# Optimization experiments

Hardware: AMD Instinct MI355X
Metric: run time of the kernel (lower is better)

Reference implementation:

```python
import jax, jax.numpy as jnp
import numpy as np
import math

E = 1024      # embed_dim
H = 16        # num_heads
HD = E // H   # head_dim
NBITS = 8


def fake_quant(x, n_bits=NBITS):
    """Symmetric per-tensor fake quantize with STE (clamp/round/dequant)."""
    qmax = 2.0 ** (n_bits - 1) - 1.0
    qmin = -(2.0 ** (n_bits - 1))
    scale = jnp.maximum(jnp.max(jnp.abs(x)) / qmax, 1e-8)
    xq = jnp.round(jnp.clip(x / scale, qmin, qmax)) * scale
    return x + jax.lax.stop_gradient(xq - x)


def setup_inputs() -> dict:
    key = jax.random.key(0)
    ks = jax.random.split(key, 7)
    L, B = 2048, 2
    query = jax.random.normal(ks[0], (L, B, E), dtype=jnp.float32)
    k_in = jax.random.normal(ks[1], (L, B, E), dtype=jnp.float32)
    v_in = jax.random.normal(ks[2], (L, B, E), dtype=jnp.float32)
    in_w = jax.random.normal(ks[3], (3 * E, E), dtype=jnp.float32) * (1.0 / math.sqrt(E))
    in_b = jax.random.normal(ks[4], (3 * E,), dtype=jnp.float32) * 0.01
    out_w = jax.random.normal(ks[5], (E, E), dtype=jnp.float32) * (1.0 / math.sqrt(E))
    out_b = jax.random.normal(ks[6], (E,), dtype=jnp.float32) * 0.01
    return {"query": query, "key": k_in, "value": v_in,
            "in_w": in_w, "in_b": in_b, "out_w": out_w, "out_b": out_b}


def reference(query, key, value, in_w, in_b, out_w, out_b):
    # NOTE: the original module ignores `key`/`value` (pure self-attention on query),
    # and its attn / softmax fake-quant lines are dead statements (results discarded).
    L, B, _ = query.shape
    Wi = fake_quant(in_w)
    Wo = fake_quant(out_w)
    # input projection: [L,B,3E]
    X = jnp.einsum('lbe,fe->lbf', query, Wi) + in_b
    X = fake_quant(X)
    Q, K, V = jnp.split(X, 3, axis=-1)  # each [L,B,E]
    # [L, B*H, HD] -> [B*H, L, HD]
    q = Q.reshape(L, B * H, HD).transpose(1, 0, 2)
    k = K.reshape(L, B * H, HD).transpose(1, 0, 2)
    v = V.reshape(L, B * H, HD).transpose(1, 0, 2)
    q = q / math.sqrt(HD)
    q = fake_quant(q)
    attn = jnp.einsum('bqd,bkd->bqk', q, k)          # [B*H, L, L]
    attn = jax.nn.softmax(attn, axis=-1)
    heads = jnp.einsum('bqk,bkd->bqd', attn, v)      # [B*H, L, HD]
    heads = fake_quant(heads)
    # [B*H, L, HD] -> [L, B*H, HD] -> [L*B, E]
    heads_r = heads.transpose(1, 0, 2).reshape(L * B, E)
    y = heads_r @ Wo.T + out_b
    y = y.reshape(L, B, E)
    return fake_quant(y)
```

## Files before the change

kernel.cpp:

```cpp
#include <hip/hip_runtime.h>
#include <math.h>

#define L_SEQ 2048
#define BATCH 2
#define EMB 1024
#define NH 16
#define HDIM 64
#define F3 3072
#define NROWS 4096

typedef __bf16 bf16_t;
typedef short s16x8 __attribute__((ext_vector_type(8)));
typedef float f32x4 __attribute__((ext_vector_type(4)));

#define MFMA16(a, b, c) __builtin_amdgcn_mfma_f32_16x16x32_bf16(a, b, c, 0, 0, 0)


__device__ __forceinline__ float u2f(unsigned u) { return __uint_as_float(u); }

__device__ __forceinline__ float max3f(float a, float b, float c) {
  return fmaxf(fmaxf(a, b), c);
}

__device__ __forceinline__ void gload16(const bf16_t* g, bf16_t* lds) {
  __builtin_amdgcn_global_load_lds((const __attribute__((address_space(1))) void*)g,
                                   (__attribute__((address_space(3))) void*)lds, 16, 0, 0);
}

__device__ __forceinline__ void blockmax_commit(float m, unsigned* slot) {
  #pragma unroll
  for (int o = 1; o < 64; o <<= 1) m = fmaxf(m, __shfl_xor(m, o));
  __shared__ float sm_[4];
  if ((threadIdx.x & 63) == 0) sm_[threadIdx.x >> 6] = m;
  __syncthreads();
  if (threadIdx.x == 0) {
    float mm = fmaxf(fmaxf(sm_[0], sm_[1]), fmaxf(sm_[2], sm_[3]));
    atomicMax(slot, __float_as_uint(mm));
  }
}

__global__ __launch_bounds__(256) void wabsmax_k(const float* __restrict__ wi,
                                                 const float* __restrict__ wo,
                                                 unsigned* __restrict__ slots) {
  float m0 = 0.0f, m1 = 0.0f;
  const int n0 = F3 * EMB / 4, n1 = EMB * EMB / 4;
  for (int i = blockIdx.x * blockDim.x + threadIdx.x; i < n0; i += gridDim.x * blockDim.x) {
    float4 v = ((const float4*)wi)[i];
    m0 = fmaxf(m0, fmaxf(fmaxf(fabsf(v.x), fabsf(v.y)), fmaxf(fabsf(v.z), fabsf(v.w))));
  }
  for (int i = blockIdx.x * blockDim.x + threadIdx.x; i < n1; i += gridDim.x * blockDim.x) {
    float4 v = ((const float4*)wo)[i];
    m1 = fmaxf(m1, fmaxf(fmaxf(fabsf(v.x), fabsf(v.y)), fmaxf(fabsf(v.z), fabsf(v.w))));
  }
  blockmax_commit(m0, slots + 0);
  blockmax_commit(m1, slots + 1);
}

__global__ __launch_bounds__(256) void prep_k(const float* __restrict__ wi,
                                              const float* __restrict__ wo,
                                              const float* __restrict__ query,
                                              bf16_t* __restrict__ Wi_int,
                                              bf16_t* __restrict__ Wo_int,
                                              bf16_t* __restrict__ q_hi,
                                              bf16_t* __restrict__ q_lo,
                                              const unsigned* __restrict__ slots) {
  float s0 = fmaxf(u2f(slots[0]) / 127.0f, 1e-8f);
  float s1 = fmaxf(u2f(slots[1]) / 127.0f, 1e-8f);
  const int n0 = F3 * EMB / 4, n1 = EMB * EMB / 4, n2 = NROWS * EMB / 4;
  for (int i = blockIdx.x * blockDim.x + threadIdx.x; i < n0; i += gridDim.x * blockDim.x) {
    float4 v = ((const float4*)wi)[i];
    bf16_t o[4];
    o[0] = (bf16_t)rintf(fminf(fmaxf(v.x / s0, -128.0f), 127.0f));
    o[1] = (bf16_t)rintf(fminf(fmaxf(v.y / s0, -128.0f), 127.0f));
    o[2] = (bf16_t)rintf(fminf(fmaxf(v.z / s0, -128.0f), 127.0f));
    o[3] = (bf16_t)rintf(fminf(fmaxf(v.w / s0, -128.0f), 127.0f));
    *(uint2*)&Wi_int[(size_t)i * 4] = *(uint2*)o;
  }
  for (int i = blockIdx.x * blockDim.x + threadIdx.x; i < n1; i += gridDim.x * blockDim.x) {
    float4 v = ((const float4*)wo)[i];
    bf16_t o[4];
    o[0] = (bf16_t)rintf(fminf(fmaxf(v.x / s1, -128.0f), 127.0f));
    o[1] = (bf16_t)rintf(fminf(fmaxf(v.y / s1, -128.0f), 127.0f));
    o[2] = (bf16_t)rintf(fminf(fmaxf(v.z / s1, -128.0f), 127.0f));
    o[3] = (bf16_t)rintf(fminf(fmaxf(v.w / s1, -128.0f), 127.0f));
    *(uint2*)&Wo_int[(size_t)i * 4] = *(uint2*)o;
  }
  for (int i = blockIdx.x * blockDim.x + threadIdx.x; i < n2; i += gridDim.x * blockDim.x) {
    float4 v = ((const float4*)query)[i];
    bf16_t h[4], l[4];
    float vv[4] = {v.x, v.y, v.z, v.w};
    #pragma unroll
    for (int j = 0; j < 4; ++j) {
      h[j] = (bf16_t)vv[j];
      l[j] = (bf16_t)(vv[j] - (float)h[j]);
    }
    *(uint2*)&q_hi[(size_t)i * 4] = *(uint2*)h;
    *(uint2*)&q_lo[(size_t)i * 4] = *(uint2*)l;
  }
}

__global__ __launch_bounds__(256) void qxv_k(const float* __restrict__ x,
                                             bf16_t* __restrict__ y,
                                             bf16_t* __restrict__ Vt,
                                             unsigned* __restrict__ slots) {
  float s = fmaxf(u2f(slots[2]) / 127.0f, 1e-8f);
  if (blockIdx.x < 2048) {
    float qm = 0.0f;
    const int n8 = NROWS * 256;
    for (int i = blockIdx.x * 256 + threadIdx.x; i < n8; i += 2048 * 256) {
      int row = i >> 8, ch = i & 255;
      const float* px = x + (size_t)row * F3 + ch * 8;
      float4 v0 = *(const float4*)px;
      float4 v1 = *(const float4*)(px + 4);
      float vv[8] = {v0.x, v0.y, v0.z, v0.w, v1.x, v1.y, v1.z, v1.w};
      bf16_t o[8];
      float lm = 0.0f;
      #pragma unroll
      for (int j = 0; j < 8; ++j) {
        float q = rintf(fminf(fmaxf(vv[j] / s, -128.0f), 127.0f));
        o[j] = (bf16_t)q;
        lm = fmaxf(lm, fabsf(q));
      }
      if (ch < 128) qm = fmaxf(qm, lm);
      *(uint4*)&y[(size_t)row * F3 + ch * 8] = *(uint4*)o;
    }
    blockmax_commit(qm, slots + 3);
  } else {
    __shared__ __align__(16) bf16_t tile[64][72];
    int vb = blockIdx.x - 2048;
    int tt = vb & 31, bh = vb >> 5;
    int b = bh >> 4, h = bh & 15;
    int t = threadIdx.x;
    #pragma unroll
    for (int i = 0; i < 2; ++i) {
      int s_ = t + i * 256;
      int tok = s_ >> 3, seg = s_ & 7;
      const float* px = x + ((size_t)(tt * 64 + tok) * BATCH + b) * F3 + 2 * EMB + h * HDIM + seg * 8;
      float4 v0 = *(const float4*)px;
      float4 v1 = *(const float4*)(px + 4);
      float vv[8] = {v0.x, v0.y, v0.z, v0.w, v1.x, v1.y, v1.z, v1.w};
      bf16_t o[8];
      #pragma unroll
      for (int j = 0; j < 8; ++j)
        o[j] = (bf16_t)rintf(fminf(fmaxf(vv[j] / s, -128.0f), 127.0f));
      int segs = seg ^ (tok >> 3);
      *(uint4*)&tile[tok][segs * 8] = *(uint4*)o;
    }
    __syncthreads();
    #pragma unroll
    for (int i = 0; i < 2; ++i) {
      int s_ = t + i * 256;
      int d = s_ >> 3, tseg = s_ & 7;
      bf16_t o[8];
      #pragma unroll
      for (int e = 0; e < 8; ++e) {
        int tok = tseg * 8 + e;
        o[e] = tile[tok][(((d >> 3) ^ (tok >> 3)) << 3) | (d & 7)];
      }
      *(uint4*)&Vt[((size_t)bh * HDIM + d) * L_SEQ + tt * 64 + tseg * 8] = *(uint4*)o;
    }
  }
}

__global__ __launch_bounds__(256) void quant_k(float* __restrict__ x, int n4,
                                               const unsigned* __restrict__ slots, int sloti) {
  float s = fmaxf(u2f(slots[sloti]) / 127.0f, 1e-8f);
  float4* x4 = (float4*)x;
  for (int i = blockIdx.x * blockDim.x + threadIdx.x; i < n4; i += gridDim.x * blockDim.x) {
    float4 v = x4[i];
    v.x = rintf(fminf(fmaxf(v.x / s, -128.0f), 127.0f)) * s;
    v.y = rintf(fminf(fmaxf(v.y / s, -128.0f), 127.0f)) * s;
    v.z = rintf(fminf(fmaxf(v.z / s, -128.0f), 127.0f)) * s;
    v.w = rintf(fminf(fmaxf(v.w / s, -128.0f), 127.0f)) * s;
    x4[i] = v;
  }
}

__global__ __launch_bounds__(256) void quantf_k(const float* __restrict__ x,
                                                bf16_t* __restrict__ y, int n4,
                                                const unsigned* __restrict__ slots, int sloti) {
  float s = fmaxf(u2f(slots[sloti]) / 127.0f, 1e-8f);
  const float4* x4 = (const float4*)x;
  for (int i = blockIdx.x * blockDim.x + threadIdx.x; i < n4; i += gridDim.x * blockDim.x) {
    float4 v = x4[i];
    bf16_t o[4];
    o[0] = (bf16_t)rintf(fminf(fmaxf(v.x / s, -128.0f), 127.0f));
    o[1] = (bf16_t)rintf(fminf(fmaxf(v.y / s, -128.0f), 127.0f));
    o[2] = (bf16_t)rintf(fminf(fmaxf(v.z / s, -128.0f), 127.0f));
    o[3] = (bf16_t)rintf(fminf(fmaxf(v.w / s, -128.0f), 127.0f));
    *(uint2*)&y[(size_t)i * 4] = *(uint2*)o;
  }
}

template <int NPARTS>
__global__ __launch_bounds__(256) void gemm_bt_mfma_k(const bf16_t* __restrict__ A0,
                                                      const bf16_t* __restrict__ A1,
                                                      const bf16_t* __restrict__ Bm,
                                                      const float* __restrict__ bias,
                                                      float* __restrict__ C,
                                                      int M, int N, int K,
                                                      unsigned* __restrict__ slots,
                                                      int sa, int sb, int smax) {
  __shared__ __align__(16) bf16_t sbuf[2][NPARTS + 1][128][32];
  int t = threadIdx.x;
  int w = t >> 6, l = t & 63, c15 = l & 15, g = l >> 4;
  int wr = w >> 1, wc = w & 1;
  int nx = gridDim.x;
  int fid = blockIdx.y * nx + blockIdx.x;
  int qq = (nx * gridDim.y) >> 3;
  int swz = (fid & 7) * qq + (fid >> 3);
  int bm = (swz / nx) * 128, bn = (swz % nx) * 128;
  f32x4 acc[4][4] = {};

  auto stage = [&](int bf, int k0) {
    #pragma unroll
    for (int i = 0; i < 2; ++i) {
      int c = i * 256 + t;
      int row = c >> 2, sg = c & 3;
      int wb = (i * 256 + w * 64) * 8;
      gload16(&A0[(size_t)(bm + row) * K + k0 + sg * 8], &sbuf[bf][0][0][0] + wb);
      if (NPARTS == 2)
        gload16(&A1[(size_t)(bm + row) * K + k0 + sg * 8], &sbuf[bf][1][0][0] + wb);
      gload16(&Bm[(size_t)(bn + row) * K + k0 + sg * 8], &sbuf[bf][NPARTS][0][0] + wb);
    }
  };

  stage(0, 0);
  __syncthreads();
  const int nk = K / 32;
  for (int kt = 0; kt < nk; ++kt) {
    int cur = kt & 1;
    if (kt + 1 < nk) stage(cur ^ 1, (kt + 1) * 32);
    s16x8 af[NPARTS][4], bf_[4];
    #pragma unroll
    for (int rt = 0; rt < 4; ++rt) {
      af[0][rt] = *(const s16x8*)&sbuf[cur][0][wr * 64 + rt * 16 + c15][g * 8];
      if (NPARTS == 2) af[1][rt] = *(const s16x8*)&sbuf[cur][1][wr * 64 + rt * 16 + c15][g * 8];
    }
    #pragma unroll
    for (int ct = 0; ct < 4; ++ct)
      bf_[ct] = *(const s16x8*)&sbuf[cur][NPARTS][wc * 64 + ct * 16 + c15][g * 8];
    __builtin_amdgcn_s_setprio(1);
    #pragma unroll
    for (int rt = 0; rt < 4; ++rt)
      #pragma unroll
      for (int ct = 0; ct < 4; ++ct) {
        acc[rt][ct] = MFMA16(af[0][rt], bf_[ct], acc[rt][ct]);
        if (NPARTS == 2) acc[rt][ct] = MFMA16(af[1][rt], bf_[ct], acc[rt][ct]);
      }
    __builtin_amdgcn_s_setprio(0);
    __syncthreads();
  }

  float s = 1.0f;
  if (sa >= 0) s *= fmaxf(u2f(slots[sa]) / 127.0f, 1e-8f);
  if (sb >= 0) s *= fmaxf(u2f(slots[sb]) / 127.0f, 1e-8f);
  float vmax = 0.0f;
  #pragma unroll
  for (int rt = 0; rt < 4; ++rt)
    #pragma unroll
    for (int r = 0; r < 4; ++r) {
      int row = bm + wr * 64 + rt * 16 + 4 * g + r;
      #pragma unroll
      for (int ct = 0; ct < 4; ++ct) {
        int col = bn + wc * 64 + ct * 16 + c15;
        float o = acc[rt][ct][r] * s + bias[col];
        vmax = fmaxf(vmax, fabsf(o));
        C[(size_t)row * N + col] = o;
      }
    }
  if (smax >= 0) blockmax_commit(vmax, slots + smax);
}

__global__ __launch_bounds__(256) void gemm_m64_k(const bf16_t* __restrict__ A,
                                                  const bf16_t* __restrict__ Bm,
                                                  const float* __restrict__ bias,
                                                  float* __restrict__ C,
                                                  int M, int N, int K,
                                                  unsigned* __restrict__ slots,
                                                  int sa, int sb, int smax) {
  __shared__ __align__(16) bf16_t As[2][64][32];
  __shared__ __align__(16) bf16_t Bs[2][128][32];
  int t = threadIdx.x;
  int w = t >> 6, l = t & 63, c15 = l & 15, g = l >> 4;
  int wr = w >> 1, wc = w & 1;
  int nx = gridDim.x;
  int fid = blockIdx.y * nx + blockIdx.x;
  int qq = (nx * gridDim.y) >> 3;
  int swz = (fid & 7) * qq + (fid >> 3);
  int bm = (swz / nx) * 64, bn = (swz % nx) * 128;
  f32x4 acc[2][4] = {};

  auto stage = [&](int bf, int k0) {
    {
      int c = t;
      int row = c >> 2, sg = c & 3;
      gload16(&A[(size_t)(bm + row) * K + k0 + sg * 8], &As[bf][0][0] + (w * 64) * 8);
    }
    #pragma unroll
    for (int i = 0; i < 2; ++i) {
      int c = i * 256 + t;
      int row = c >> 2, sg = c & 3;
      gload16(&Bm[(size_t)(bn + row) * K + k0 + sg * 8],
              &Bs[bf][0][0] + (i * 256 + w * 64) * 8);
    }
  };

  stage(0, 0);
  __syncthreads();
  const int nk = K / 32;
  for (int kt = 0; kt < nk; ++kt) {
    int cur = kt & 1;
    if (kt + 1 < nk) stage(cur ^ 1, (kt + 1) * 32);
    s16x8 af[2], bf_[4];
    #pragma unroll
    for (int rt = 0; rt < 2; ++rt)
      af[rt] = *(const s16x8*)&As[cur][wr * 32 + rt * 16 + c15][g * 8];
    #pragma unroll
    for (int ct = 0; ct < 4; ++ct)
      bf_[ct] = *(const s16x8*)&Bs[cur][wc * 64 + ct * 16 + c15][g * 8];
    __builtin_amdgcn_s_setprio(1);
    #pragma unroll
    for (int rt = 0; rt < 2; ++rt)
      #pragma unroll
      for (int ct = 0; ct < 4; ++ct)
        acc[rt][ct] = MFMA16(af[rt], bf_[ct], acc[rt][ct]);
    __builtin_amdgcn_s_setprio(0);
    __syncthreads();
  }

  float s = 1.0f;
  if (sa >= 0) s *= fmaxf(u2f(slots[sa]) / 127.0f, 1e-8f);
  if (sb >= 0) s *= fmaxf(u2f(slots[sb]) / 127.0f, 1e-8f);
  float vmax = 0.0f;
  #pragma unroll
  for (int rt = 0; rt < 2; ++rt)
    #pragma unroll
    for (int r = 0; r < 4; ++r) {
      int row = bm + wr * 32 + rt * 16 + 4 * g + r;
      #pragma unroll
      for (int ct = 0; ct < 4; ++ct) {
        int col = bn + wc * 64 + ct * 16 + c15;
        float o = acc[rt][ct][r] * s + bias[col];
        vmax = fmaxf(vmax, fabsf(o));
        C[(size_t)row * N + col] = o;
      }
    }
  if (smax >= 0) blockmax_commit(vmax, slots + smax);
}

__global__ __launch_bounds__(256) void attn_mfma_k(const bf16_t* __restrict__ X,
                                                   const bf16_t* __restrict__ Vt,
                                                   float* __restrict__ heads,
                                                   unsigned* __restrict__ slots) {
  int bh = blockIdx.x, qb = blockIdx.y;
  int b = bh >> 4, h = bh & 15;
  int t = threadIdx.x;
  int w = t >> 6, l = t & 63, c15 = l & 15, g = l >> 4;

  float s_x = fmaxf(u2f(slots[2]) / 127.0f, 1e-8f);
  float s_q = fmaxf((u2f(slots[3]) * s_x) * 0.125f / 127.0f, 1e-8f);
  const float LOG2E = 1.4426950408889634f;
  float qsl2 = s_q * s_x * LOG2E;

  __shared__ __align__(16) union SmKV {
    struct { bf16_t K[2][64][64]; bf16_t V[2][64][64]; } kv;
    float Ot[4][16][69];
  } sm;

  int qrow = qb * 64 + w * 16 + c15;
  const bf16_t* qbase = X + ((size_t)qrow * BATCH + b) * F3 + h * HDIM;
  s16x8 qf0, qf1;
  {
    bf16_t qt[8];
    #pragma unroll
    for (int half = 0; half < 2; ++half) {
      *(uint4*)qt = *(const uint4*)(qbase + half * 32 + g * 8);
      #pragma unroll
      for (int j = 0; j < 8; ++j) {
        float q = ((float)qt[j] * s_x) * 0.125f;
        qt[j] = (bf16_t)rintf(fminf(fmaxf(q / s_q, -128.0f), 127.0f));
      }
      if (half == 0) qf0 = *(s16x8*)qt; else qf1 = *(s16x8*)qt;
    }
  }

  const size_t tokstride = (size_t)BATCH * F3;
  const bf16_t* kbase = X + (size_t)b * F3 + EMB + h * HDIM;
  const bf16_t* vbase = Vt + (size_t)bh * HDIM * L_SEQ;

  auto stage = [&](int buf, int kt) {
    #pragma unroll
    for (int i = 0; i < 2; ++i) {
      int c = i * 256 + t;
      int a = c >> 3, blk = c & 7;
      int kap = (a & 0x20) | ((a & 0x10) >> 2) | ((a & 0x0C) << 1) | (a & 3);
      gload16(kbase + (size_t)(kt * 64 + kap) * tokstride + (blk ^ (a & 7)) * 8,
              &sm.kv.K[buf][0][0] + (i * 256 + w * 64) * 8);
    }
    #pragma unroll
    for (int i = 0; i < 2; ++i) {
      int c = i * 256 + t;
      int d = c >> 3, blk = c & 7;
      gload16(vbase + (size_t)d * L_SEQ + kt * 64 + (blk ^ (d & 7)) * 8,
              &sm.kv.V[buf][0][0] + (i * 256 + w * 64) * 8);
    }
  };

  f32x4 acc_o[4] = {};
  float m_prev = -INFINITY, lsum = 0.0f;
  int sw = c15 & 7;

  stage(0, 0);
  __syncthreads();

  const int NT = L_SEQ / 64;
  int cur = 0;
  for (int kt = 0; kt < NT; ++kt) {
    if (kt + 1 < NT) stage(cur ^ 1, kt + 1);

    f32x4 accs[4] = {};
    __builtin_amdgcn_s_setprio(1);
    #pragma unroll
    for (int ct = 0; ct < 4; ++ct) {
      const bf16_t* krow = &sm.kv.K[cur][ct * 16 + c15][0];
      s16x8 kf0 = *(const s16x8*)(krow + (g ^ sw) * 8);
      s16x8 kf1 = *(const s16x8*)(krow + ((g | 4) ^ sw) * 8);
      accs[ct] = MFMA16(kf0, qf0, accs[ct]);
      accs[ct] = MFMA16(kf1, qf1, accs[ct]);
    }
    __builtin_amdgcn_s_setprio(0);

    float t0 = max3f(accs[0][0], accs[0][1], accs[0][2]);
    float t1 = max3f(accs[0][3], accs[1][0], accs[1][1]);
    float t2 = max3f(accs[1][2], accs[1][3], accs[2][0]);
    float t3 = max3f(accs[2][1], accs[2][2], accs[2][3]);
    float t4 = max3f(accs[3][0], accs[3][1], accs[3][2]);
    float pm = fmaxf(max3f(t0, t1, t2), max3f(t3, t4, accs[3][3]));
    pm = fmaxf(pm, __shfl_xor(pm, 16));
    pm = fmaxf(pm, __shfl_xor(pm, 32));
    float mnew = fmaxf(m_prev, pm);
    float f_ = __builtin_amdgcn_exp2f((m_prev - mnew) * qsl2);
    float mq = mnew * qsl2;
    float ps = 0.0f;
    bf16_t hh[2][8], ll[2][8];
    #pragma unroll
    for (int ct = 0; ct < 4; ++ct) {
      float p[4];
      #pragma unroll
      for (int r = 0; r < 4; ++r) p[r] = __builtin_amdgcn_exp2f(fmaf(accs[ct][r], qsl2, -mq));
      ps += (p[0] + p[1]) + (p[2] + p[3]);
      #pragma unroll
      for (int r = 0; r < 4; ++r) {
        bf16_t hi = (bf16_t)p[r];
        hh[ct >> 1][(ct & 1) * 4 + r] = hi;
        ll[ct >> 1][(ct & 1) * 4 + r] = (bf16_t)(p[r] - (float)hi);
      }
    }
    lsum = lsum * f_ + ps;
    m_prev = mnew;

    if (!__all(f_ == 1.0f)) {
      #pragma unroll
      for (int dt = 0; dt < 4; ++dt)
        #pragma unroll
        for (int r = 0; r < 4; ++r) acc_o[dt][r] *= f_;
    }

    s16x8 pfh0 = *(s16x8*)hh[0], pfh1 = *(s16x8*)hh[1];
    s16x8 pfl0 = *(s16x8*)ll[0], pfl1 = *(s16x8*)ll[1];
    __builtin_amdgcn_s_setprio(1);
    #pragma unroll
    for (int dt = 0; dt < 4; ++dt) {
      const bf16_t* vrow = &sm.kv.V[cur][dt * 16 + c15][0];
      s16x8 vf0 = *(const s16x8*)(vrow + (g ^ sw) * 8);
      s16x8 vf1 = *(const s16x8*)(vrow + ((g | 4) ^ sw) * 8);
      acc_o[dt] = MFMA16(vf0, pfh0, acc_o[dt]);
      acc_o[dt] = MFMA16(vf1, pfh1, acc_o[dt]);
      acc_o[dt] = MFMA16(vf0, pfl0, acc_o[dt]);
      acc_o[dt] = MFMA16(vf1, pfl1, acc_o[dt]);
    }
    __builtin_amdgcn_s_setprio(0);

    __syncthreads();
    cur ^= 1;
  }

  lsum += __shfl_xor(lsum, 16);
  lsum += __shfl_xor(lsum, 32);
  float inv = s_x / lsum;

  float hm = 0.0f;
  #pragma unroll
  for (int dt = 0; dt < 4; ++dt)
    #pragma unroll
    for (int r = 0; r < 4; ++r) {
      float o = acc_o[dt][r] * inv;
      hm = fmaxf(hm, fabsf(o));
      sm.Ot[w][c15][dt * 16 + 4 * g + r] = o;
    }
  int ql = l >> 2, cs = l & 3;
  #pragma unroll
  for (int j = 0; j < 4; ++j) {
    int cch = cs + 4 * j;
    float4 v = *(const float4*)&sm.Ot[w][ql][cch * 4];
    int row = qb * 64 + w * 16 + ql;
    *(float4*)&heads[((size_t)row * BATCH + b) * EMB + h * HDIM + cch * 4] = v;
  }
  blockmax_commit(hm, slots + 4);
}

extern "C" void kernel_launch(void* const* d_in, const int* in_sizes, int n_in,
                              void* d_out, int out_size, void* d_ws, size_t ws_size,
                              hipStream_t stream) {
  (void)in_sizes; (void)n_in; (void)out_size; (void)ws_size;
  const float* query = (const float*)d_in[0];
  const float* in_w  = (const float*)d_in[3];
  const float* in_b  = (const float*)d_in[4];
  const float* out_w = (const float*)d_in[5];
  const float* out_b = (const float*)d_in[6];
  float* out = (float*)d_out;

  unsigned* slots = (unsigned*)d_ws;
  char* p = (char*)d_ws + 256;
  bf16_t* q_hi   = (bf16_t*)p;                  p += (size_t)NROWS * EMB * 2;
  bf16_t* q_lo   = (bf16_t*)p;                  p += (size_t)NROWS * EMB * 2;
  bf16_t* Wi_int = (bf16_t*)p;                  p += (size_t)F3 * EMB * 2;
  bf16_t* Wo_int = (bf16_t*)p;                  p += (size_t)EMB * EMB * 2;
  float*  X_f32  = (float*)p;                   p += (size_t)NROWS * F3 * 4;
  bf16_t* X_int  = (bf16_t*)p;
  bf16_t* Vt     = q_hi;
  bf16_t* heads_int = (bf16_t*)X_f32;
  float*  heads_f32 = out;

  hipMemsetAsync(d_ws, 0, 256, stream);

  dim3 b256(256);
  wabsmax_k<<<768, b256, 0, stream>>>(in_w, out_w, slots);
  prep_k<<<1024, b256, 0, stream>>>(in_w, out_w, query, Wi_int, Wo_int, q_hi, q_lo, slots);

  gemm_bt_mfma_k<2><<<dim3(F3 / 128, NROWS / 128), b256, 0, stream>>>(
      q_hi, q_lo, Wi_int, in_b, X_f32, NROWS, F3, EMB, slots, -1, 0, 2);

  qxv_k<<<3072, b256, 0, stream>>>(X_f32, X_int, Vt, slots);

  attn_mfma_k<<<dim3(BATCH * NH, L_SEQ / 64), b256, 0, stream>>>(X_int, Vt, heads_f32, slots);

  quantf_k<<<1024, b256, 0, stream>>>(heads_f32, heads_int, NROWS * EMB / 4, slots, 4);

  gemm_m64_k<<<dim3(EMB / 128, NROWS / 64), b256, 0, stream>>>(
      heads_int, Wo_int, out_b, out, NROWS, EMB, EMB, slots, 4, 1, 5);

  quant_k<<<1024, b256, 0, stream>>>(out, NROWS * EMB / 4, slots, 5);
}
```

Before: 240.7 us.

## Switch input-projection GEMM to 32x32 MFMA with XOR-swizzled LDS layout

Replaces the 16x16x32 MFMA tiling in the input-projection GEMM with 32x32x16 bf16 MFMA, so each wave holds 2x2 accumulator tiles of 16 floats instead of 4x4 tiles of 4. The LDS staging now XOR-swizzles the 8-element k-chunk by row bits to avoid bank conflicts on fragment reads. The aim is fewer LDS reads per MFMA and higher MFMA throughput. The epilogue is rewritten to match the 32x32 output layout, and its stores are less coalesced per row.

```diff
diff --git a/kernel.cpp b/kernel.cpp
--- a/kernel.cpp
+++ b/kernel.cpp
@@ -12,8 +12,10 @@
 typedef __bf16 bf16_t;
 typedef short s16x8 __attribute__((ext_vector_type(8)));
 typedef float f32x4 __attribute__((ext_vector_type(4)));
+typedef float f32x16 __attribute__((ext_vector_type(16)));
 
 #define MFMA16(a, b, c) __builtin_amdgcn_mfma_f32_16x16x32_bf16(a, b, c, 0, 0, 0)
+#define MFMA32(a, b, c) __builtin_amdgcn_mfma_f32_32x32x16_bf16(a, b, c, 0, 0, 0)
 
 
 __device__ __forceinline__ float u2f(unsigned u) { return __uint_as_float(u); }
@@ -192,36 +194,35 @@
   }
 }
 
-template <int NPARTS>
-__global__ __launch_bounds__(256) void gemm_bt_mfma_k(const bf16_t* __restrict__ A0,
-                                                      const bf16_t* __restrict__ A1,
-                                                      const bf16_t* __restrict__ Bm,
-                                                      const float* __restrict__ bias,
-                                                      float* __restrict__ C,
-                                                      int M, int N, int K,
-                                                      unsigned* __restrict__ slots,
-                                                      int sa, int sb, int smax) {
-  __shared__ __align__(16) bf16_t sbuf[2][NPARTS + 1][128][32];
+__global__ __launch_bounds__(256) void gemm1_k(const bf16_t* __restrict__ A0,
+                                               const bf16_t* __restrict__ A1,
+                                               const bf16_t* __restrict__ Bm,
+                                               const float* __restrict__ bias,
+                                               float* __restrict__ C,
+                                               int M, int N, int K,
+                                               unsigned* __restrict__ slots,
+                                               int sa, int sb, int smax) {
+  __shared__ __align__(16) bf16_t sbuf[2][3][128][32];
   int t = threadIdx.x;
-  int w = t >> 6, l = t & 63, c15 = l & 15, g = l >> 4;
+  int w = t >> 6, l = t & 63, r32 = l & 31, half = l >> 5;
   int wr = w >> 1, wc = w & 1;
   int nx = gridDim.x;
   int fid = blockIdx.y * nx + blockIdx.x;
   int qq = (nx * gridDim.y) >> 3;
   int swz = (fid & 7) * qq + (fid >> 3);
   int bm = (swz / nx) * 128, bn = (swz % nx) * 128;
-  f32x4 acc[4][4] = {};
+  f32x16 acc[2][2] = {};
 
   auto stage = [&](int bf, int k0) {
     #pragma unroll
     for (int i = 0; i < 2; ++i) {
       int c = i * 256 + t;
-      int row = c >> 2, sg = c & 3;
+      int row = c >> 2, cc = c & 3;
+      int kk = k0 + ((cc ^ ((row >> 1) & 3)) << 3);
       int wb = (i * 256 + w * 64) * 8;
-      gload16(&A0[(size_t)(bm + row) * K + k0 + sg * 8], &sbuf[bf][0][0][0] + wb);
-      if (NPARTS == 2)
-        gload16(&A1[(size_t)(bm + row) * K + k0 + sg * 8], &sbuf[bf][1][0][0] + wb);
-      gload16(&Bm[(size_t)(bn + row) * K + k0 + sg * 8], &sbuf[bf][NPARTS][0][0] + wb);
+      gload16(&A0[(size_t)(bm + row) * K + kk], &sbuf[bf][0][0][0] + wb);
+      gload16(&A1[(size_t)(bm + row) * K + kk], &sbuf[bf][1][0][0] + wb);
+      gload16(&Bm[(size_t)(bn + row) * K + kk], &sbuf[bf][2][0][0] + wb);
     }
   };
 
@@ -231,23 +232,38 @@
   for (int kt = 0; kt < nk; ++kt) {
     int cur = kt & 1;
     if (kt + 1 < nk) stage(cur ^ 1, (kt + 1) * 32);
-    s16x8 af[NPARTS][4], bf_[4];
-    #pragma unroll
-    for (int rt = 0; rt < 4; ++rt) {
-      af[0][rt] = *(const s16x8*)&sbuf[cur][0][wr * 64 + rt * 16 + c15][g * 8];
-      if (NPARTS == 2) af[1][rt] = *(const s16x8*)&sbuf[cur][1][wr * 64 + rt * 16 + c15][g * 8];
-    }
-    #pragma unroll
-    for (int ct = 0; ct < 4; ++ct)
-      bf_[ct] = *(const s16x8*)&sbuf[cur][NPARTS][wc * 64 + ct * 16 + c15][g * 8];
+    s16x8 a0f[2][2], a1f[2][2], bf_[2][2];
+    #pragma unroll
+    for (int rt = 0; rt < 2; ++rt) {
+      int row = wr * 64 + rt * 32 + r32;
+      int sz = (row >> 1) & 3;
+      #pragma unroll
+      for (int kc = 0; kc < 2; ++kc) {
+        int ch = ((kc << 1) | half) ^ sz;
+        a0f[rt][kc] = *(const s16x8*)&sbuf[cur][0][row][ch * 8];
+        a1f[rt][kc] = *(const s16x8*)&sbuf[cur][1][row][ch * 8];
+      }
+    }
+    #pragma unroll
+    for (int ct = 0; ct < 2; ++ct) {
+      int row = wc * 64 + ct * 32 + r32;
+      int sz = (row >> 1) & 3;
+      #pragma unroll
+      for (int kc = 0; kc < 2; ++kc) {
+        int ch = ((kc << 1) | half) ^ sz;
+        bf_[ct][kc] = *(const s16x8*)&sbuf[cur][2][row][ch * 8];
+      }
+    }
     __builtin_amdgcn_s_setprio(1);
     #pragma unroll
-    for (int rt = 0; rt < 4; ++rt)
-      #pragma unroll
-      for (int ct = 0; ct < 4; ++ct) {
-        acc[rt][ct] = MFMA16(af[0][rt], bf_[ct], acc[rt][ct]);
-        if (NPARTS == 2) acc[rt][ct] = MFMA16(af[1][rt], bf_[ct], acc[rt][ct]);
-      }
+    for (int rt = 0; rt < 2; ++rt)
+      #pragma unroll
+      for (int ct = 0; ct < 2; ++ct)
+        #pragma unroll
+        for (int kc = 0; kc < 2; ++kc) {
+          acc[rt][ct] = MFMA32(a0f[rt][kc], bf_[ct][kc], acc[rt][ct]);
+          acc[rt][ct] = MFMA32(a1f[rt][kc], bf_[ct][kc], acc[rt][ct]);
+        }
     __builtin_amdgcn_s_setprio(0);
     __syncthreads();
   }
@@ -257,17 +273,20 @@
   if (sb >= 0) s *= fmaxf(u2f(slots[sb]) / 127.0f, 1e-8f);
   float vmax = 0.0f;
   #pragma unroll
-  for (int rt = 0; rt < 4; ++rt)
-    #pragma unroll
-    for (int r = 0; r < 4; ++r) {
-      int row = bm + wr * 64 + rt * 16 + 4 * g + r;
-      #pragma unroll
-      for (int ct = 0; ct < 4; ++ct) {
-        int col = bn + wc * 64 + ct * 16 + c15;
-        float o = acc[rt][ct][r] * s + bias[col];
-        vmax = fmaxf(vmax, fabsf(o));
-        C[(size_t)row * N + col] = o;
-      }
+  for (int rt = 0; rt < 2; ++rt)
+    #pragma unroll
+    for (int ct = 0; ct < 2; ++ct) {
+      int col = bn + wc * 64 + ct * 32 + r32;
+      float b_ = bias[col];
+      #pragma unroll
+      for (int q = 0; q < 4; ++q)
+        #pragma unroll
+        for (int r = 0; r < 4; ++r) {
+          int row = bm + wr * 64 + rt * 32 + q * 8 + r + 4 * half;
+          float o = acc[rt][ct][q * 4 + r] * s + b_;
+          vmax = fmaxf(vmax, fabsf(o));
+          C[(size_t)row * N + col] = o;
+        }
     }
   if (smax >= 0) blockmax_commit(vmax, slots + smax);
 }
@@ -539,7 +558,7 @@
   wabsmax_k<<<768, b256, 0, stream>>>(in_w, out_w, slots);
   prep_k<<<1024, b256, 0, stream>>>(in_w, out_w, query, Wi_int, Wo_int, q_hi, q_lo, slots);
 
-  gemm_bt_mfma_k<2><<<dim3(F3 / 128, NROWS / 128), b256, 0, stream>>>(
+  gemm1_k<<<dim3(F3 / 128, NROWS / 128), b256, 0, stream>>>(
       q_hi, q_lo, Wi_int, in_b, X_f32, NROWS, F3, EMB, slots, -1, 0, 2);
 
   qxv_k<<<3072, b256, 0, stream>>>(X_f32, X_int, Vt, slots);
```

After: 264.7 us. +10.0%, slower.

## Use 512-thread blocks with split load roles for split-precision input projection GEMM

Applied to the files above, without the earlier changes.

The input projection GEMM moves from 256 to 512 threads per 128x128 tile. Each wave now owns a 64x32 sub-tile instead of 64x64, which halves the accumulator registers per wave. The global-to-LDS loads are split between wave groups: waves 0-3 stage the A0 and B operands and waves 4-7 stage A1. This is meant to raise the number of waves per CU and hide latency better, at the cost of more LDS reads of A fragments, since each A fragment is now read by four waves rather than two.

```diff
diff --git a/kernel.cpp b/kernel.cpp
--- a/kernel.cpp
+++ b/kernel.cpp
@@ -30,11 +30,13 @@
 __device__ __forceinline__ void blockmax_commit(float m, unsigned* slot) {
   #pragma unroll
   for (int o = 1; o < 64; o <<= 1) m = fmaxf(m, __shfl_xor(m, o));
-  __shared__ float sm_[4];
+  __shared__ float sm_[8];
+  int nw = blockDim.x >> 6;
   if ((threadIdx.x & 63) == 0) sm_[threadIdx.x >> 6] = m;
   __syncthreads();
   if (threadIdx.x == 0) {
-    float mm = fmaxf(fmaxf(sm_[0], sm_[1]), fmaxf(sm_[2], sm_[3]));
+    float mm = sm_[0];
+    for (int i = 1; i < nw; ++i) mm = fmaxf(mm, sm_[i]);
     atomicMax(slot, __float_as_uint(mm));
   }
 }
@@ -192,36 +194,44 @@
   }
 }
 
-template <int NPARTS>
-__global__ __launch_bounds__(256) void gemm_bt_mfma_k(const bf16_t* __restrict__ A0,
-                                                      const bf16_t* __restrict__ A1,
-                                                      const bf16_t* __restrict__ Bm,
-                                                      const float* __restrict__ bias,
-                                                      float* __restrict__ C,
-                                                      int M, int N, int K,
-                                                      unsigned* __restrict__ slots,
-                                                      int sa, int sb, int smax) {
-  __shared__ __align__(16) bf16_t sbuf[2][NPARTS + 1][128][32];
+__global__ __launch_bounds__(512) void gemm1_k(const bf16_t* __restrict__ A0,
+                                               const bf16_t* __restrict__ A1,
+                                               const bf16_t* __restrict__ Bm,
+                                               const float* __restrict__ bias,
+                                               float* __restrict__ C,
+                                               int M, int N, int K,
+                                               unsigned* __restrict__ slots,
+                                               int sa, int sb, int smax) {
+  __shared__ __align__(16) bf16_t sbuf[2][3][128][32];
   int t = threadIdx.x;
   int w = t >> 6, l = t & 63, c15 = l & 15, g = l >> 4;
-  int wr = w >> 1, wc = w & 1;
+  int wr = w >> 2, wc = w & 3;
   int nx = gridDim.x;
   int fid = blockIdx.y * nx + blockIdx.x;
   int qq = (nx * gridDim.y) >> 3;
   int swz = (fid & 7) * qq + (fid >> 3);
   int bm = (swz / nx) * 128, bn = (swz % nx) * 128;
-  f32x4 acc[4][4] = {};
+  f32x4 acc[4][2] = {};
 
   auto stage = [&](int bf, int k0) {
-    #pragma unroll
-    for (int i = 0; i < 2; ++i) {
-      int c = i * 256 + t;
-      int row = c >> 2, sg = c & 3;
-      int wb = (i * 256 + w * 64) * 8;
-      gload16(&A0[(size_t)(bm + row) * K + k0 + sg * 8], &sbuf[bf][0][0][0] + wb);
-      if (NPARTS == 2)
+    if (w < 4) {
+      #pragma unroll
+      for (int i = 0; i < 2; ++i) {
+        int c = i * 256 + w * 64 + l;
+        int row = c >> 2, sg = c & 3;
+        int wb = (i * 256 + w * 64) * 8;
+        gload16(&A0[(size_t)(bm + row) * K + k0 + sg * 8], &sbuf[bf][0][0][0] + wb);
+        gload16(&Bm[(size_t)(bn + row) * K + k0 + sg * 8], &sbuf[bf][2][0][0] + wb);
+      }
+    } else {
+      int w4 = w - 4;
+      #pragma unroll
+      for (int i = 0; i < 2; ++i) {
+        int c = i * 256 + w4 * 64 + l;
+        int row = c >> 2, sg = c & 3;
+        int wb = (i * 256 + w4 * 64) * 8;
         gload16(&A1[(size_t)(bm + row) * K + k0 + sg * 8], &sbuf[bf][1][0][0] + wb);
-      gload16(&Bm[(size_t)(bn + row) * K + k0 + sg * 8], &sbuf[bf][NPARTS][0][0] + wb);
+      }
     }
   };
 
@@ -231,22 +241,23 @@
   for (int kt = 0; kt < nk; ++kt) {
     int cur = kt & 1;
     if (kt + 1 < nk) stage(cur ^ 1, (kt + 1) * 32);
-    s16x8 af[NPARTS][4], bf_[4];
+    s16x8 a0f[4], a1f[4], bf_[2];
     #pragma unroll
     for (int rt = 0; rt < 4; ++rt) {
-      af[0][rt] = *(const s16x8*)&sbuf[cur][0][wr * 64 + rt * 16 + c15][g * 8];
-      if (NPARTS == 2) af[1][rt] = *(const s16x8*)&sbuf[cur][1][wr * 64 + rt * 16 + c15][g * 8];
-    }
-    #pragma unroll
-    for (int ct = 0; ct < 4; ++ct)
-      bf_[ct] = *(const s16x8*)&sbuf[cur][NPARTS][wc * 64 + ct * 16 + c15][g * 8];
+      int row = wr * 64 + rt * 16 + c15;
+      a0f[rt] = *(const s16x8*)&sbuf[cur][0][row][g * 8];
+      a1f[rt] = *(const s16x8*)&sbuf[cur][1][row][g * 8];
+    }
+    #pragma unroll
+    for (int ct = 0; ct < 2; ++ct)
+      bf_[ct] = *(const s16x8*)&sbuf[cur][2][wc * 32 + ct * 16 + c15][g * 8];
     __builtin_amdgcn_s_setprio(1);
     #pragma unroll
     for (int rt = 0; rt < 4; ++rt)
       #pragma unroll
-      for (int ct = 0; ct < 4; ++ct) {
-        acc[rt][ct] = MFMA16(af[0][rt], bf_[ct], acc[rt][ct]);
-        if (NPARTS == 2) acc[rt][ct] = MFMA16(af[1][rt], bf_[ct], acc[rt][ct]);
+      for (int ct = 0; ct < 2; ++ct) {
+        acc[rt][ct] = MFMA16(a0f[rt], bf_[ct], acc[rt][ct]);
+        acc[rt][ct] = MFMA16(a1f[rt], bf_[ct], acc[rt][ct]);
       }
     __builtin_amdgcn_s_setprio(0);
     __syncthreads();
@@ -262,8 +273,8 @@
     for (int r = 0; r < 4; ++r) {
       int row = bm + wr * 64 + rt * 16 + 4 * g + r;
       #pragma unroll
-      for (int ct = 0; ct < 4; ++ct) {
-        int col = bn + wc * 64 + ct * 16 + c15;
+      for (int ct = 0; ct < 2; ++ct) {
+        int col = bn + wc * 32 + ct * 16 + c15;
         float o = acc[rt][ct][r] * s + bias[col];
         vmax = fmaxf(vmax, fabsf(o));
         C[(size_t)row * N + col] = o;
@@ -539,7 +550,7 @@
   wabsmax_k<<<768, b256, 0, stream>>>(in_w, out_w, slots);
   prep_k<<<1024, b256, 0, stream>>>(in_w, out_w, query, Wi_int, Wo_int, q_hi, q_lo, slots);
 
-  gemm_bt_mfma_k<2><<<dim3(F3 / 128, NROWS / 128), b256, 0, stream>>>(
+  gemm1_k<<<dim3(F3 / 128, NROWS / 128), dim3(512), 0, stream>>>(
       q_hi, q_lo, Wi_int, in_b, X_f32, NROWS, F3, EMB, slots, -1, 0, 2);
 
   qxv_k<<<3072, b256, 0, stream>>>(X_f32, X_int, Vt, slots);
```

Result: slower. 264.5 us (+9.9%).
